# Optimization experiments

Hardware: AMD Instinct MI355X
Metric: run time of the kernel (lower is better)

## Reference

```python
import jax, jax.numpy as jnp
import numpy as np

B, T, D = 4096, 200, 64
H1, H2 = 80, 40
C = 64  # cate_count


def setup_inputs() -> dict:
    key = jax.random.key(0)
    ks = jax.random.split(key, 12)
    q = jax.random.normal(ks[0], (B, D), dtype=jnp.float32)
    k = jax.random.normal(ks[1], (B, T, D), dtype=jnp.float32)
    mask = jax.random.randint(ks[2], (B, T), 0, 2, dtype=jnp.int32)
    hist_cate = jax.random.randint(ks[3], (B, T), 0, C, dtype=jnp.int32)
    # attention MLP params (Dense(80, PReLU), Dense(40, PReLU), Dense(1))
    W1 = jax.random.normal(ks[4], (4 * D, H1), dtype=jnp.float32) * (1.0 / np.sqrt(4 * D))
    b1 = jnp.zeros((H1,), dtype=jnp.float32)
    a1 = jnp.full((H1,), 0.25, dtype=jnp.float32)  # PReLU slopes
    W2 = jax.random.normal(ks[5], (H1, H2), dtype=jnp.float32) * (1.0 / np.sqrt(H1))
    b2 = jnp.zeros((H2,), dtype=jnp.float32)
    a2 = jnp.full((H2,), 0.25, dtype=jnp.float32)
    Wf = jax.random.normal(ks[6], (H2, 1), dtype=jnp.float32) * (1.0 / np.sqrt(H2))
    bf = jnp.zeros((1,), dtype=jnp.float32)
    return {
        "q": q, "k": k, "mask": mask, "hist_cate": hist_cate,
        "cate_count": C,
        "W1": W1, "b1": b1, "a1": a1,
        "W2": W2, "b2": b2, "a2": a2,
        "Wf": Wf, "bf": bf,
    }


def _prelu(x, alpha):
    return jnp.maximum(x, 0.0) + alpha * jnp.minimum(x, 0.0)


def reference(q, k, mask, hist_cate, cate_count, W1, b1, a1, W2, b2, a2, Wf, bf):
    b, t, d = k.shape
    qe = jnp.broadcast_to(q[:, None, :], (b, t, d))          # tile q over seq
    info = jnp.concatenate([qe, k, qe - k, qe * k], axis=-1)  # [B,T,4D]
    h = _prelu(info @ W1 + b1, a1)                            # [B,T,H1]
    h = _prelu(h @ W2 + b2, a2)                               # [B,T,H2]
    logits = (h @ Wf + bf)[..., 0]                            # [B,T]
    neg = jnp.float32(-2 ** 32 + 1)
    logits = jnp.where(mask == 0, neg, logits)
    logits = logits / jnp.sqrt(jnp.float32(d))
    w = jax.nn.softmax(logits, axis=-1)                       # [B,T]
    user_interest = jnp.einsum('bt,btd->bd', w, k)            # [B,D]
    # fused per-category masked weighted pooling (replaces Python loop)
    onehot = (hist_cate[:, None, :] == jnp.arange(cate_count, dtype=hist_cate.dtype)[None, :, None])  # [B,C,T]
    wc = w[:, None, :] * onehot.astype(w.dtype)               # [B,C,T]
    wc = wc / (jnp.sum(wc, axis=-1, keepdims=True) + 1e-10)
    cate_hidden = jnp.einsum('bct,btd->bcd', wc, k)           # [B,C,D]
    return user_interest, cate_hidden
```

## Files before the change

### kernel.cpp

```cpp
#include <hip/hip_runtime.h>

typedef unsigned short u16;
typedef short short8 __attribute__((ext_vector_type(8)));
typedef float f32x4 __attribute__((ext_vector_type(4)));

#define NEG_MASK -4294967295.0f

__device__ __forceinline__ u16 f2bf(float f) {
    unsigned int x = __float_as_uint(f);
    unsigned int r = (x + 0x7FFFu + ((x >> 16) & 1u)) >> 16;
    return (u16)r;
}
__device__ __forceinline__ short8 cvt8(float4 a, float4 b) {
    union { short8 v; u16 u[8]; } r;
    r.u[0] = f2bf(a.x); r.u[1] = f2bf(a.y); r.u[2] = f2bf(a.z); r.u[3] = f2bf(a.w);
    r.u[4] = f2bf(b.x); r.u[5] = f2bf(b.y); r.u[6] = f2bf(b.z); r.u[7] = f2bf(b.w);
    return r.v;
}

__global__ __launch_bounds__(256, 4) void din_kernel(
    const float* __restrict__ qp, const float* __restrict__ kp,
    const int* __restrict__ maskp, const int* __restrict__ catep,
    const float* __restrict__ W1p, const float* __restrict__ b1p,
    const float* __restrict__ a1p, const float* __restrict__ W2p,
    const float* __restrict__ b2p, const float* __restrict__ a2p,
    const float* __restrict__ wfp, const float* __restrict__ bfp,
    float* __restrict__ outp)
{
    __shared__ __align__(16) u16 MtW2t[80*72 + 48*104];
    __shared__ __align__(16) u16 H1p[4*16*104];
    __shared__ float logits_s[200];
    __shared__ float q_s[64], qW_s[80], a1_s[80];
    __shared__ float a2_s[48], b2_s[48], wf_s[48];
    __shared__ float s_c[64], red_s[8], bf_s;
    __shared__ int cate_s[200];
    __shared__ int mask_s[200];

    u16* Mt  = MtW2t;
    u16* W2t = MtW2t + 80*72;
    float* cate_acc = (float*)MtW2t;
    float* qW2 = logits_s;

    const int tid  = threadIdx.x;
    const int b    = blockIdx.x;
    const int wid  = tid >> 6;
    const int lane = tid & 63;
    const int i16  = lane & 15;
    const int q4   = lane >> 4;
    const float* kb = kp + (size_t)b * 12800;

    {
        unsigned int* w2z = (unsigned int*)W2t;
        for (int i = tid; i < (48*104)/2; i += 256) w2z[i] = 0u;
    }
    for (int i = tid; i < 4*16*12; i += 256) {
        int buf = i / 192, rem = i % 192, row = rem / 12, j = rem % 12;
        *(unsigned int*)&H1p[buf*(16*104) + row*104 + 80 + j*2] = 0u;
    }
    if (tid < 64) { s_c[tid] = 0.f; q_s[tid] = qp[(size_t)b*64 + tid]; }
    if (tid < 48) {
        wf_s[tid] = (tid < 40) ? wfp[tid] : 0.f;
        a2_s[tid] = (tid < 40) ? a2p[tid] : 0.f;
        b2_s[tid] = (tid < 40) ? b2p[tid] : 0.f;
    }
    if (tid < 80) a1_s[tid] = a1p[tid];
    if (tid == 0) bf_s = bfp[0];
    if (tid < 200) {
        cate_s[tid] = catep[(size_t)b*200 + tid];
        mask_s[tid] = maskp[(size_t)b*200 + tid];
    }
    __syncthreads();

    #pragma unroll 4
    for (int j = tid; j < 5120; j += 256) {
        int d = j / 80, h = j - d*80;
        float m = W1p[5120 + j] - W1p[10240 + j] + q_s[d] * W1p[15360 + j];
        Mt[h*72 + d] = f2bf(m);
    }
    if (tid < 160) {
        int p = tid / 80, h = tid - p*80;
        float acc0 = 0.f, acc1 = 0.f;
        int d0 = p * 32;
        #pragma unroll 4
        for (int d = d0; d < d0 + 32; d += 2) {
            acc0 += q_s[d]   * (W1p[d*80 + h]     + W1p[(128+d)*80 + h]);
            acc1 += q_s[d+1] * (W1p[(d+1)*80 + h] + W1p[(129+d)*80 + h]);
        }
        qW2[tid] = acc0 + acc1;
    }
    #pragma unroll 4
    for (int e = tid; e < 3200; e += 256) {
        int n = e % 40, kk = e / 40;
        W2t[n*104 + kk] = f2bf(W2p[e]);
    }
    __syncthreads();
    if (tid < 80) qW_s[tid] = b1p[tid] + qW2[tid] + qW2[80 + tid];
    __syncthreads();

    u16* hb = &H1p[wid * (16*104)];
    {
        int mt = wid;
        float4 f0, f1, f2, f3;
        {
            int arow = mt*16 + i16; if (arow > 199) arow = 199;
            const float4* kr = (const float4*)(kb + arow*64);
            f0 = kr[2*q4];     f1 = kr[2*q4 + 1];
            f2 = kr[8 + 2*q4]; f3 = kr[9 + 2*q4];
        }
        for (; mt < 13; mt += 4) {
            int nmt = mt + 4; if (nmt > 12) nmt = 12;
            int narow = nmt*16 + i16; if (narow > 199) narow = 199;
            const float4* nkr = (const float4*)(kb + narow*64);
            float4 g0 = nkr[2*q4],     g1 = nkr[2*q4 + 1];
            float4 g2 = nkr[8 + 2*q4], g3 = nkr[9 + 2*q4];

            short8 ka0 = cvt8(f0, f1);
            short8 ka1 = cvt8(f2, f3);
            #pragma unroll
            for (int nt = 0; nt < 5; ++nt) {
                int n0 = nt*16;
                float qwv = qW_s[n0 + i16];
                f32x4 acc = { qwv, qwv, qwv, qwv };
                short8 b0 = *(const short8*)&Mt[(n0+i16)*72 + q4*8];
                short8 b1 = *(const short8*)&Mt[(n0+i16)*72 + 32 + q4*8];
                acc = __builtin_amdgcn_mfma_f32_16x16x32_bf16(ka0, b0, acc, 0, 0, 0);
                acc = __builtin_amdgcn_mfma_f32_16x16x32_bf16(ka1, b1, acc, 0, 0, 0);
                float al = a1_s[n0 + i16];
                #pragma unroll
                for (int r = 0; r < 4; ++r) {
                    float x = acc[r];
                    float y = (x > 0.f) ? x : al * x;
                    hb[(q4*4 + r)*104 + n0 + i16] = f2bf(y);
                }
            }
            short8 A0 = *(const short8*)&hb[i16*104 + q4*8];
            short8 A1 = *(const short8*)&hb[i16*104 + 32 + q4*8];
            short8 A2 = *(const short8*)&hb[i16*104 + 64 + q4*8];
            float part0 = 0.f, part1 = 0.f, part2 = 0.f, part3 = 0.f;
            #pragma unroll
            for (int nt = 0; nt < 3; ++nt) {
                int n0 = nt*16;
                float b2v = b2_s[n0 + i16];
                f32x4 acc = { b2v, b2v, b2v, b2v };
                short8 w0 = *(const short8*)&W2t[(n0+i16)*104 + q4*8];
                short8 w1 = *(const short8*)&W2t[(n0+i16)*104 + 32 + q4*8];
                short8 w2 = *(const short8*)&W2t[(n0+i16)*104 + 64 + q4*8];
                acc = __builtin_amdgcn_mfma_f32_16x16x32_bf16(A0, w0, acc, 0, 0, 0);
                acc = __builtin_amdgcn_mfma_f32_16x16x32_bf16(A1, w1, acc, 0, 0, 0);
                acc = __builtin_amdgcn_mfma_f32_16x16x32_bf16(A2, w2, acc, 0, 0, 0);
                float al2 = a2_s[n0 + i16];
                float wfv = wf_s[n0 + i16];
                float x, y;
                x = acc[0]; y = (x > 0.f) ? x : al2*x; part0 += y*wfv;
                x = acc[1]; y = (x > 0.f) ? x : al2*x; part1 += y*wfv;
                x = acc[2]; y = (x > 0.f) ? x : al2*x; part2 += y*wfv;
                x = acc[3]; y = (x > 0.f) ? x : al2*x; part3 += y*wfv;
            }
            #pragma unroll
            for (int off = 1; off < 16; off <<= 1) {
                part0 += __shfl_xor(part0, off, 64);
                part1 += __shfl_xor(part1, off, 64);
                part2 += __shfl_xor(part2, off, 64);
                part3 += __shfl_xor(part3, off, 64);
            }
            if (i16 == 0) {
                float p0[4] = { part0, part1, part2, part3 };
                #pragma unroll
                for (int r = 0; r < 4; ++r) {
                    int t = mt*16 + q4*4 + r;
                    if (t < 200) {
                        int mv = mask_s[t];
                        float v = (mv == 0) ? NEG_MASK : (bf_s + p0[r]);
                        logits_s[t] = v * 0.125f;
                    }
                }
            }
            f0 = g0; f1 = g1; f2 = g2; f3 = g3;
        }
    }
    __syncthreads();

    {
        float4 z = {0.f, 0.f, 0.f, 0.f};
        float4* ca4 = (float4*)cate_acc;
        for (int i = tid; i < 1024; i += 256) ca4[i] = z;
    }
    const int t0 = wid * 50;
    float kd[10];
    #pragma unroll
    for (int j = 0; j < 10; ++j) kd[j] = kb[(t0 + j)*64 + lane];

    float x = (tid < 200) ? logits_s[tid] : -3.0e38f;
    float m = x;
    #pragma unroll
    for (int off = 32; off >= 1; off >>= 1) m = fmaxf(m, __shfl_xor(m, off, 64));
    if (lane == 0) red_s[wid] = m;
    __syncthreads();
    float mx = fmaxf(fmaxf(red_s[0], red_s[1]), fmaxf(red_s[2], red_s[3]));
    float e = (tid < 200) ? __expf(x - mx) : 0.f;
    float s = e;
    #pragma unroll
    for (int off = 32; off >= 1; off >>= 1) s += __shfl_xor(s, off, 64);
    if (lane == 0) red_s[4 + wid] = s;
    __syncthreads();
    float tot = red_s[4] + red_s[5] + red_s[6] + red_s[7];
    float wv = e / tot;
    if (tid < 200) {
        logits_s[tid] = wv;
        if (wv > 0.f) atomicAdd(&s_c[cate_s[tid]], wv);
    }
    __syncthreads();

    for (int i = 0; i < 50; i += 10) {
        float nkd[10];
        const bool more = (i + 10 < 50);
        if (more) {
            #pragma unroll
            for (int j = 0; j < 10; ++j) nkd[j] = kb[(t0 + i + 10 + j)*64 + lane];
        }
        float w_[10]; int c_[10];
        #pragma unroll
        for (int j = 0; j < 10; ++j) { w_[j] = logits_s[t0+i+j]; c_[j] = cate_s[t0+i+j]; }
        #pragma unroll
        for (int j = 0; j < 10; ++j) {
            float w = w_[j];
            if (w > 0.f) atomicAdd(&cate_acc[c_[j]*64 + lane], w * kd[j]);
        }
        if (more) {
            #pragma unroll
            for (int j = 0; j < 10; ++j) kd[j] = nkd[j];
        }
    }
    __syncthreads();

    if (tid < 64) {
        float ui = 0.f;
        #pragma unroll 8
        for (int c = 0; c < 64; ++c) ui += cate_acc[c*64 + tid];
        outp[(size_t)b*64 + tid] = ui;
    }
    {
        float* outc = outp + (size_t)(4096*64) + (size_t)b*4096;
        #pragma unroll
        for (int ii = 0; ii < 4; ++ii) {
            int i = tid*4 + ii*1024;
            float inv = 1.0f / (s_c[i >> 6] + 1e-10f);
            float4 v = *(const float4*)&cate_acc[i];
            v.x *= inv; v.y *= inv; v.z *= inv; v.w *= inv;
            *(float4*)&outc[i] = v;
        }
    }
}

extern "C" void kernel_launch(void* const* d_in, const int* in_sizes, int n_in,
                              void* d_out, int out_size, void* d_ws, size_t ws_size,
                              hipStream_t stream) {
    din_kernel<<<4096, 256, 0, stream>>>(
        (const float*)d_in[0],
        (const float*)d_in[1],
        (const int*)d_in[2],
        (const int*)d_in[3],
        (const float*)d_in[5],
        (const float*)d_in[6],
        (const float*)d_in[7],
        (const float*)d_in[8],
        (const float*)d_in[9],
        (const float*)d_in[10],
        (const float*)d_in[11],
        (const float*)d_in[12],
        (float*)d_out);
}
```

Measured before the change: 573.7 us.

## Keep layer-1 activations in registers via transposed MFMA and lane shuffles

Measured after the change: 705.4 us. 1.23x slower.

```diff
diff --git a/kernel.cpp b/kernel.cpp
--- a/kernel.cpp
+++ b/kernel.cpp
@@ -18,7 +18,7 @@
     return r.v;
 }
 
-__global__ __launch_bounds__(256, 4) void din_kernel(
+__global__ __launch_bounds__(256, 6) void din_kernel(
     const float* __restrict__ qp, const float* __restrict__ kp,
     const int* __restrict__ maskp, const int* __restrict__ catep,
     const float* __restrict__ W1p, const float* __restrict__ b1p,
@@ -28,10 +28,9 @@
     float* __restrict__ outp)
 {
     __shared__ __align__(16) u16 MtW2t[80*72 + 48*104];
-    __shared__ __align__(16) u16 H1p[4*16*104];
-    __shared__ float logits_s[200];
-    __shared__ float q_s[64], qW_s[80], a1_s[80];
-    __shared__ float a2_s[48], b2_s[48], wf_s[48];
+    __shared__ __align__(16) float logits_s[200];
+    __shared__ __align__(16) float q_s[64], qW_s[80], a1_s[80];
+    __shared__ __align__(16) float a2_s[48], b2_s[48], wf_s[48];
     __shared__ float s_c[64], red_s[8], bf_s;
     __shared__ int cate_s[200];
     __shared__ int mask_s[200];
@@ -52,10 +51,6 @@
     {
         unsigned int* w2z = (unsigned int*)W2t;
         for (int i = tid; i < (48*104)/2; i += 256) w2z[i] = 0u;
-    }
-    for (int i = tid; i < 4*16*12; i += 256) {
-        int buf = i / 192, rem = i % 192, row = rem / 12, j = rem % 12;
-        *(unsigned int*)&H1p[buf*(16*104) + row*104 + 80 + j*2] = 0u;
     }
     if (tid < 64) { s_c[tid] = 0.f; q_s[tid] = qp[(size_t)b*64 + tid]; }
     if (tid < 48) {
@@ -97,7 +92,6 @@
     if (tid < 80) qW_s[tid] = b1p[tid] + qW2[tid] + qW2[80 + tid];
     __syncthreads();
 
-    u16* hb = &H1p[wid * (16*104)];
     {
         int mt = wid;
         float4 f0, f1, f2, f3;
@@ -107,75 +101,91 @@
             f0 = kr[2*q4];     f1 = kr[2*q4 + 1];
             f2 = kr[8 + 2*q4]; f3 = kr[9 + 2*q4];
         }
+        const int srcA = i16 + ((lane & 16) << 1);
+        const int srcB = srcA + 16;
+        const bool hi4 = (q4 >> 1) != 0;
         for (; mt < 13; mt += 4) {
-            int nmt = mt + 4; if (nmt > 12) nmt = 12;
-            int narow = nmt*16 + i16; if (narow > 199) narow = 199;
-            const float4* nkr = (const float4*)(kb + narow*64);
-            float4 g0 = nkr[2*q4],     g1 = nkr[2*q4 + 1];
-            float4 g2 = nkr[8 + 2*q4], g3 = nkr[9 + 2*q4];
-
             short8 ka0 = cvt8(f0, f1);
             short8 ka1 = cvt8(f2, f3);
+            {
+                int nmt = mt + 4; if (nmt > 12) nmt = 12;
+                int narow = nmt*16 + i16; if (narow > 199) narow = 199;
+                const float4* nkr = (const float4*)(kb + narow*64);
+                f0 = nkr[2*q4];     f1 = nkr[2*q4 + 1];
+                f2 = nkr[8 + 2*q4]; f3 = nkr[9 + 2*q4];
+            }
+            unsigned int P0[2], P1[2], P2[2], P3[2], P4[2];
+#define G1(nt, Pd) { \
+            const int n0 = (nt)*16; \
+            float4 qw4 = *(const float4*)&qW_s[n0 + q4*4]; \
+            f32x4 acc = { qw4.x, qw4.y, qw4.z, qw4.w }; \
+            short8 m0 = *(const short8*)&Mt[(n0+i16)*72 + q4*8]; \
+            short8 m1 = *(const short8*)&Mt[(n0+i16)*72 + 32 + q4*8]; \
+            acc = __builtin_amdgcn_mfma_f32_16x16x32_bf16(m0, ka0, acc, 0, 0, 0); \
+            acc = __builtin_amdgcn_mfma_f32_16x16x32_bf16(m1, ka1, acc, 0, 0, 0); \
+            float4 al4 = *(const float4*)&a1_s[n0 + q4*4]; \
+            float y0 = (acc[0] > 0.f) ? acc[0] : al4.x * acc[0]; \
+            float y1 = (acc[1] > 0.f) ? acc[1] : al4.y * acc[1]; \
+            float y2 = (acc[2] > 0.f) ? acc[2] : al4.z * acc[2]; \
+            float y3 = (acc[3] > 0.f) ? acc[3] : al4.w * acc[3]; \
+            Pd[0] = (unsigned int)f2bf(y0) | ((unsigned int)f2bf(y1) << 16); \
+            Pd[1] = (unsigned int)f2bf(y2) | ((unsigned int)f2bf(y3) << 16); }
+            G1(0, P0) G1(1, P1) G1(2, P2) G1(3, P3) G1(4, P4)
+#undef G1
+            union BW { unsigned int w[4]; short8 v; } B0, B1, B2;
+            {
+                int xa, xb, ya, yb, za, zb, wa, wb;
+                xa = __shfl((int)P0[0], srcA); xb = __shfl((int)P0[1], srcA);
+                ya = __shfl((int)P0[0], srcB); yb = __shfl((int)P0[1], srcB);
+                za = __shfl((int)P1[0], srcA); zb = __shfl((int)P1[1], srcA);
+                wa = __shfl((int)P1[0], srcB); wb = __shfl((int)P1[1], srcB);
+                B0.w[0] = hi4 ? (unsigned)za : (unsigned)xa;
+                B0.w[1] = hi4 ? (unsigned)zb : (unsigned)xb;
+                B0.w[2] = hi4 ? (unsigned)wa : (unsigned)ya;
+                B0.w[3] = hi4 ? (unsigned)wb : (unsigned)yb;
+                xa = __shfl((int)P2[0], srcA); xb = __shfl((int)P2[1], srcA);
+                ya = __shfl((int)P2[0], srcB); yb = __shfl((int)P2[1], srcB);
+                za = __shfl((int)P3[0], srcA); zb = __shfl((int)P3[1], srcA);
+                wa = __shfl((int)P3[0], srcB); wb = __shfl((int)P3[1], srcB);
+                B1.w[0] = hi4 ? (unsigned)za : (unsigned)xa;
+                B1.w[1] = hi4 ? (unsigned)zb : (unsigned)xb;
+                B1.w[2] = hi4 ? (unsigned)wa : (unsigned)ya;
+                B1.w[3] = hi4 ? (unsigned)wb : (unsigned)yb;
+                xa = __shfl((int)P4[0], srcA); xb = __shfl((int)P4[1], srcA);
+                ya = __shfl((int)P4[0], srcB); yb = __shfl((int)P4[1], srcB);
+                B2.w[0] = hi4 ? 0u : (unsigned)xa;
+                B2.w[1] = hi4 ? 0u : (unsigned)xb;
+                B2.w[2] = hi4 ? 0u : (unsigned)ya;
+                B2.w[3] = hi4 ? 0u : (unsigned)yb;
+            }
+            float part = 0.f;
             #pragma unroll
-            for (int nt = 0; nt < 5; ++nt) {
-                int n0 = nt*16;
-                float qwv = qW_s[n0 + i16];
-                f32x4 acc = { qwv, qwv, qwv, qwv };
-                short8 b0 = *(const short8*)&Mt[(n0+i16)*72 + q4*8];
-                short8 b1 = *(const short8*)&Mt[(n0+i16)*72 + 32 + q4*8];
-                acc = __builtin_amdgcn_mfma_f32_16x16x32_bf16(ka0, b0, acc, 0, 0, 0);
-                acc = __builtin_amdgcn_mfma_f32_16x16x32_bf16(ka1, b1, acc, 0, 0, 0);
-                float al = a1_s[n0 + i16];
-                #pragma unroll
-                for (int r = 0; r < 4; ++r) {
-                    float x = acc[r];
-                    float y = (x > 0.f) ? x : al * x;
-                    hb[(q4*4 + r)*104 + n0 + i16] = f2bf(y);
+            for (int gt = 0; gt < 3; ++gt) {
+                const int g0 = gt*16;
+                float4 b24 = *(const float4*)&b2_s[g0 + q4*4];
+                f32x4 acc = { b24.x, b24.y, b24.z, b24.w };
+                short8 w0 = *(const short8*)&W2t[(g0+i16)*104 + q4*8];
+                short8 w1 = *(const short8*)&W2t[(g0+i16)*104 + 32 + q4*8];
+                short8 w2 = *(const short8*)&W2t[(g0+i16)*104 + 64 + q4*8];
+                acc = __builtin_amdgcn_mfma_f32_16x16x32_bf16(w0, B0.v, acc, 0, 0, 0);
+                acc = __builtin_amdgcn_mfma_f32_16x16x32_bf16(w1, B1.v, acc, 0, 0, 0);
+                acc = __builtin_amdgcn_mfma_f32_16x16x32_bf16(w2, B2.v, acc, 0, 0, 0);
+                float4 a24 = *(const float4*)&a2_s[g0 + q4*4];
+                float4 wf4 = *(const float4*)&wf_s[g0 + q4*4];
+                part += ((acc[0] > 0.f) ? acc[0] : a24.x * acc[0]) * wf4.x;
+                part += ((acc[1] > 0.f) ? acc[1] : a24.y * acc[1]) * wf4.y;
+                part += ((acc[2] > 0.f) ? acc[2] : a24.z * acc[2]) * wf4.z;
+                part += ((acc[3] > 0.f) ? acc[3] : a24.w * acc[3]) * wf4.w;
+            }
+            part += __shfl_xor(part, 16, 64);
+            part += __shfl_xor(part, 32, 64);
+            if (lane < 16) {
+                int t = mt*16 + lane;
+                if (t < 200) {
+                    float v = (mask_s[t] == 0) ? NEG_MASK : (bf_s + part);
+                    logits_s[t] = v * 0.125f;
                 }
             }
-            short8 A0 = *(const short8*)&hb[i16*104 + q4*8];
-            short8 A1 = *(const short8*)&hb[i16*104 + 32 + q4*8];
-            short8 A2 = *(const short8*)&hb[i16*104 + 64 + q4*8];
-            float part0 = 0.f, part1 = 0.f, part2 = 0.f, part3 = 0.f;
-            #pragma unroll
-            for (int nt = 0; nt < 3; ++nt) {
-                int n0 = nt*16;
-                float b2v = b2_s[n0 + i16];
-                f32x4 acc = { b2v, b2v, b2v, b2v };
-                short8 w0 = *(const short8*)&W2t[(n0+i16)*104 + q4*8];
-                short8 w1 = *(const short8*)&W2t[(n0+i16)*104 + 32 + q4*8];
-                short8 w2 = *(const short8*)&W2t[(n0+i16)*104 + 64 + q4*8];
-                acc = __builtin_amdgcn_mfma_f32_16x16x32_bf16(A0, w0, acc, 0, 0, 0);
-                acc = __builtin_amdgcn_mfma_f32_16x16x32_bf16(A1, w1, acc, 0, 0, 0);
-                acc = __builtin_amdgcn_mfma_f32_16x16x32_bf16(A2, w2, acc, 0, 0, 0);
-                float al2 = a2_s[n0 + i16];
-                float wfv = wf_s[n0 + i16];
-                float x, y;
-                x = acc[0]; y = (x > 0.f) ? x : al2*x; part0 += y*wfv;
-                x = acc[1]; y = (x > 0.f) ? x : al2*x; part1 += y*wfv;
-                x = acc[2]; y = (x > 0.f) ? x : al2*x; part2 += y*wfv;
-                x = acc[3]; y = (x > 0.f) ? x : al2*x; part3 += y*wfv;
-            }
-            #pragma unroll
-            for (int off = 1; off < 16; off <<= 1) {
-                part0 += __shfl_xor(part0, off, 64);
-                part1 += __shfl_xor(part1, off, 64);
-                part2 += __shfl_xor(part2, off, 64);
-                part3 += __shfl_xor(part3, off, 64);
-            }
-            if (i16 == 0) {
-                float p0[4] = { part0, part1, part2, part3 };
-                #pragma unroll
-                for (int r = 0; r < 4; ++r) {
-                    int t = mt*16 + q4*4 + r;
-                    if (t < 200) {
-                        int mv = mask_s[t];
-                        float v = (mv == 0) ? NEG_MASK : (bf_s + p0[r]);
-                        logits_s[t] = v * 0.125f;
-                    }
-                }
-            }
-            f0 = g0; f1 = g1; f2 = g2; f3 = g3;
         }
     }
     __syncthreads();
```
